# Optimization experiments

Measured on AMD Instinct MI355X. Metric: run time of the kernel, lower is better.

Reference implementation:

```python
import jax, jax.numpy as jnp
import numpy as np

TOKENS, DIM, DIM_OUT, R, ALPHA = 8192, 4096, 4096, 16, 32
SCALE = ALPHA / R  # 2.0


def setup_inputs() -> dict:
    key = jax.random.key(0)
    k1, k2, k3, k4, k5 = jax.random.split(key, 5)
    x = jax.random.normal(k1, (TOKENS, DIM), dtype=jnp.float32)
    A = jax.random.normal(k2, (DIM, R), dtype=jnp.float32)
    B = jax.random.normal(k3, (R, DIM_OUT), dtype=jnp.float32) * 0.02
    W = jax.random.normal(k4, (DIM_OUT, DIM), dtype=jnp.float32) * 0.02  # base Linear weight
    b = jax.random.normal(k5, (DIM_OUT,), dtype=jnp.float32)
    return {"x": x, "A": A, "B": B, "W": W, "b": b}


def reference(x, A, B, W, b):
    # LoRA path: x @ (A @ B) * scale, computed in the efficient low-rank order
    # (mathematically identical to materializing the full-rank weight).
    lora = ((x @ A) @ B) * SCALE              # [tokens, dim_out]
    base = x @ W.T + b                         # wrapped base Linear forward
    return lora + base
```

## Files before the change

kernel.cpp:

```cpp
#include <hip/hip_runtime.h>
#include <hip/hip_bf16.h>
#include <stdint.h>

#define TOKENS   8192
#define DIM      4096
#define DIM_OUT  4096
#define LORA_R   16
#define LORA_SCALE 2.0f

typedef __bf16 bf16_t;
typedef __attribute__((ext_vector_type(8))) __bf16 bfrag;
typedef __attribute__((ext_vector_type(4))) float f32x4;

__device__ __forceinline__ void gload_lds16(const bf16_t* gsrc, bf16_t* ldst) {
    __builtin_amdgcn_global_load_lds(
        (const __attribute__((address_space(1))) uint32_t*)(const void*)gsrc,
        (__attribute__((address_space(3))) uint32_t*)(void*)ldst,
        16, 0, 0);
}

#define CAST_BLOCKS 2048
__global__ void prep_kernel(const float* __restrict__ x, bf16_t* __restrict__ xb,
                            const float* __restrict__ W, const float* __restrict__ A,
                            const float* __restrict__ B, bf16_t* __restrict__ Wt) {
    if (blockIdx.x < CAST_BLOCKS) {
        const int total = TOKENS * DIM / 8;
        for (int i = blockIdx.x * blockDim.x + threadIdx.x; i < total;
             i += CAST_BLOCKS * 256) {
            const float4* p = reinterpret_cast<const float4*>(x + (size_t)i * 8);
            float4 v0 = p[0], v1 = p[1];
            union { bf16_t o[8]; uint4 u; } pk;
            pk.o[0] = (bf16_t)v0.x; pk.o[1] = (bf16_t)v0.y;
            pk.o[2] = (bf16_t)v0.z; pk.o[3] = (bf16_t)v0.w;
            pk.o[4] = (bf16_t)v1.x; pk.o[5] = (bf16_t)v1.y;
            pk.o[6] = (bf16_t)v1.z; pk.o[7] = (bf16_t)v1.w;
            *reinterpret_cast<uint4*>(xb + (size_t)i * 8) = pk.u;
        }
    } else {
        int idx = (blockIdx.x - CAST_BLOCKS) * blockDim.x + threadIdx.x;
        int k0 = (idx & 511) << 3;
        int n0 = (idx >> 9) << 2;

        float bn[4][16];
#pragma unroll
        for (int r = 0; r < 16; ++r) {
            float4 bv = *reinterpret_cast<const float4*>(B + (size_t)r * DIM_OUT + n0);
            bn[0][r] = bv.x; bn[1][r] = bv.y; bn[2][r] = bv.z; bn[3][r] = bv.w;
        }
        float ab[4][8];
#pragma unroll
        for (int j = 0; j < 8; ++j) {
            const float4* ap = reinterpret_cast<const float4*>(A + (size_t)(k0 + j) * LORA_R);
            float4 a0 = ap[0], a1 = ap[1], a2 = ap[2], a3 = ap[3];
            float av[16] = {a0.x,a0.y,a0.z,a0.w,a1.x,a1.y,a1.z,a1.w,
                            a2.x,a2.y,a2.z,a2.w,a3.x,a3.y,a3.z,a3.w};
#pragma unroll
            for (int n = 0; n < 4; ++n) {
                float s = 0.f;
#pragma unroll
                for (int r = 0; r < 16; ++r) s += av[r] * bn[n][r];
                ab[n][j] = s;
            }
        }
#pragma unroll
        for (int n = 0; n < 4; ++n) {
            const float4* wp = reinterpret_cast<const float4*>(W + (size_t)(n0 + n) * DIM + k0);
            float4 w0 = wp[0], w1 = wp[1];
            float wv[8] = {w0.x,w0.y,w0.z,w0.w,w1.x,w1.y,w1.z,w1.w};
            union { bf16_t o[8]; uint4 u; } pk;
#pragma unroll
            for (int j = 0; j < 8; ++j) pk.o[j] = (bf16_t)(wv[j] + LORA_SCALE * ab[n][j]);
            *reinterpret_cast<uint4*>(Wt + (size_t)(n0 + n) * DIM + k0) = pk.u;
        }
    }
}

#define BM 256
#define BN 256
#define BK 64
#define MB_BLKS (TOKENS / BM)
#define NB_BLKS (DIM_OUT / BN)
#define NT      (DIM / BK)

#define SB0() __builtin_amdgcn_sched_barrier(0)
#define VMWAIT_(n) asm volatile("s_waitcnt vmcnt(" #n ")" ::: "memory")
#define VMWAIT(n) VMWAIT_(n)
#define TILEBAR() do { SB0(); VMWAIT(0); __builtin_amdgcn_s_barrier(); SB0(); } while (0)

__global__ __launch_bounds__(512, 2) void gemm_kernel(
    const bf16_t* __restrict__ Xb, const bf16_t* __restrict__ Wt,
    const float* __restrict__ bias, float* __restrict__ C)
{
    __shared__ __align__(16) bf16_t sA[2][BM][BK];
    __shared__ __align__(16) bf16_t sB[2][BN][BK];

    const int nwg = MB_BLKS * NB_BLKS;
    int bid = blockIdx.x;
    int swz = (bid & 7) * (nwg >> 3) + (bid >> 3);
    int bm = swz / NB_BLKS;
    int bn = swz % NB_BLKS;

    const int tid  = threadIdx.x;
    const int lane = tid & 63;
    const int wid  = tid >> 6;
    const int wr   = wid >> 2;
    const int wc   = wid & 3;

    const int srow = tid >> 3;
    const int scol = (tid & 7) * 8;
    const int koff = (((tid & 7) ^ ((tid >> 3) & 7)) * 8);
    const bf16_t* Ag = Xb + (size_t)(bm * BM + srow) * DIM + koff;
    const bf16_t* Bg = Wt + (size_t)(bn * BN + srow) * DIM + koff;

#define STAGE_A(dd, kt) do { \
    const bf16_t* s_ = Ag + (size_t)(kt) * BK; \
    bf16_t* d_ = &sA[dd][srow][scol]; \
    gload_lds16(s_,                     d_); \
    gload_lds16(s_ + (size_t)64  * DIM, d_ + 64  * BK); \
    gload_lds16(s_ + (size_t)128 * DIM, d_ + 128 * BK); \
    gload_lds16(s_ + (size_t)192 * DIM, d_ + 192 * BK); \
} while (0)

#define STAGE_B(dd, kt) do { \
    const bf16_t* s_ = Bg + (size_t)(kt) * BK; \
    bf16_t* d_ = &sB[dd][srow][scol]; \
    gload_lds16(s_,                     d_); \
    gload_lds16(s_ + (size_t)64  * DIM, d_ + 64  * BK); \
    gload_lds16(s_ + (size_t)128 * DIM, d_ + 128 * BK); \
    gload_lds16(s_ + (size_t)192 * DIM, d_ + 192 * BK); \
} while (0)

    const int q     = lane & 7;
    const int kslot = lane >> 4;
    const int r15   = lane & 15;
    const int cK0   = ((kslot    ) ^ q) * 8;
    const int cK1   = ((kslot + 4) ^ q) * 8;
    const int arow0 = wr * 128 + r15;
    const int brow0 = wc * 64  + r15;

    f32x4 acc[8][4] = {};
    bfrag aLo[4][2], aHi[4][2], bLo[2][2], bHi[2][2];

#define READ_A4(dst, dd, mb) do { \
    _Pragma("unroll") \
    for (int m_ = 0; m_ < 4; ++m_) { \
        dst[m_][0] = *reinterpret_cast<const bfrag*>(&sA[dd][arow0 + (mb + m_) * 16][cK0]); \
        dst[m_][1] = *reinterpret_cast<const bfrag*>(&sA[dd][arow0 + (mb + m_) * 16][cK1]); \
    } \
} while (0)

#define READ_B2(dst, dd, nb) do { \
    _Pragma("unroll") \
    for (int n_ = 0; n_ < 2; ++n_) { \
        dst[n_][0] = *reinterpret_cast<const bfrag*>(&sB[dd][brow0 + (nb + n_) * 16][cK0]); \
        dst[n_][1] = *reinterpret_cast<const bfrag*>(&sB[dd][brow0 + (nb + n_) * 16][cK1]); \
    } \
} while (0)

#define MFMA_Q(Af, Bf, mb, nb) do { \
    __builtin_amdgcn_s_setprio(1); \
    _Pragma("unroll") \
    for (int m_ = 0; m_ < 4; ++m_) \
    _Pragma("unroll") \
    for (int n_ = 0; n_ < 2; ++n_) \
    _Pragma("unroll") \
    for (int ks_ = 0; ks_ < 2; ++ks_) \
        acc[mb + m_][nb + n_] = __builtin_amdgcn_mfma_f32_16x16x32_bf16( \
            Af[m_][ks_], Bf[n_][ks_], acc[mb + m_][nb + n_], 0, 0, 0); \
    __builtin_amdgcn_s_setprio(0); \
} while (0)

#define TILE1(d, ktn, S) do { \
    if (S) { STAGE_A((d) ^ 1, ktn); STAGE_B((d) ^ 1, ktn); } \
    READ_A4(aLo, d, 0); READ_B2(bLo, d, 0); READ_B2(bHi, d, 2); READ_A4(aHi, d, 4); \
    MFMA_Q(aLo, bLo, 0, 0); MFMA_Q(aLo, bHi, 0, 2); \
    MFMA_Q(aHi, bHi, 4, 2); MFMA_Q(aHi, bLo, 4, 0); \
    TILEBAR(); \
} while (0)

    STAGE_A(0, 0); STAGE_B(0, 0);
    TILEBAR();

    for (int it = 0; it < NT / 2 - 1; ++it) {
        int t = 2 * it;
        TILE1(0, t + 1, true);
        TILE1(1, t + 2, true);
    }
    TILE1(0, 63, true);
    TILE1(1, 0, false);

    int row0 = bm * BM + wr * 128 + (lane >> 4) * 4;
    int col0 = bn * BN + wc * 64 + r15;
#pragma unroll
    for (int n = 0; n < 4; ++n) {
        int c = col0 + n * 16;
        float bv = bias[c];
#pragma unroll
        for (int m = 0; m < 8; ++m) {
            int r = row0 + m * 16;
#pragma unroll
            for (int j = 0; j < 4; ++j)
                C[(size_t)(r + j) * DIM_OUT + c] = acc[m][n][j] + bv;
        }
    }
}

extern "C" void kernel_launch(void* const* d_in, const int* in_sizes, int n_in,
                              void* d_out, int out_size, void* d_ws, size_t ws_size,
                              hipStream_t stream) {
    const float* x = (const float*)d_in[0];
    const float* A = (const float*)d_in[1];
    const float* B = (const float*)d_in[2];
    const float* W = (const float*)d_in[3];
    const float* b = (const float*)d_in[4];
    float* out = (float*)d_out;

    bf16_t* xb = (bf16_t*)d_ws;
    bf16_t* Wt = (bf16_t*)((char*)d_ws + (size_t)TOKENS * DIM * 2);

    prep_kernel<<<CAST_BLOCKS + 2048, 256, 0, stream>>>(x, xb, W, A, B, Wt);
    gemm_kernel<<<MB_BLKS * NB_BLKS, 512, 0, stream>>>(xb, Wt, b, out);
}
```

Measured before the change: 335.7 us.

## Use BK=32 with four LDS buffers and partial vmcnt waits

```diff
diff --git a/kernel.cpp b/kernel.cpp
--- a/kernel.cpp
+++ b/kernel.cpp
@@ -77,7 +77,7 @@
 
 #define BM 256
 #define BN 256
-#define BK 64
+#define BK 32
 #define MB_BLKS (TOKENS / BM)
 #define NB_BLKS (DIM_OUT / BN)
 #define NT      (DIM / BK)
@@ -85,14 +85,13 @@
 #define SB0() __builtin_amdgcn_sched_barrier(0)
 #define VMWAIT_(n) asm volatile("s_waitcnt vmcnt(" #n ")" ::: "memory")
 #define VMWAIT(n) VMWAIT_(n)
-#define TILEBAR() do { SB0(); VMWAIT(0); __builtin_amdgcn_s_barrier(); SB0(); } while (0)
 
 __global__ __launch_bounds__(512, 2) void gemm_kernel(
     const bf16_t* __restrict__ Xb, const bf16_t* __restrict__ Wt,
     const float* __restrict__ bias, float* __restrict__ C)
 {
-    __shared__ __align__(16) bf16_t sA[2][BM][BK];
-    __shared__ __align__(16) bf16_t sB[2][BN][BK];
+    __shared__ __align__(16) bf16_t sA[4][BM][BK];
+    __shared__ __align__(16) bf16_t sB[4][BN][BK];
 
     const int nwg = MB_BLKS * NB_BLKS;
     int bid = blockIdx.x;
@@ -106,88 +105,68 @@
     const int wr   = wid >> 2;
     const int wc   = wid & 3;
 
-    const int srow = tid >> 3;
-    const int scol = (tid & 7) * 8;
-    const int koff = (((tid & 7) ^ ((tid >> 3) & 7)) * 8);
+    const int srow = tid >> 2;
+    const int slin = (tid & 3) * 8;
+    const int koff = (((tid & 3) ^ ((tid >> 3) & 3)) * 8);
     const bf16_t* Ag = Xb + (size_t)(bm * BM + srow) * DIM + koff;
     const bf16_t* Bg = Wt + (size_t)(bn * BN + srow) * DIM + koff;
 
-#define STAGE_A(dd, kt) do { \
+#define STAGE_A(sb, kt) do { \
     const bf16_t* s_ = Ag + (size_t)(kt) * BK; \
-    bf16_t* d_ = &sA[dd][srow][scol]; \
-    gload_lds16(s_,                     d_); \
-    gload_lds16(s_ + (size_t)64  * DIM, d_ + 64  * BK); \
-    gload_lds16(s_ + (size_t)128 * DIM, d_ + 128 * BK); \
-    gload_lds16(s_ + (size_t)192 * DIM, d_ + 192 * BK); \
+    gload_lds16(s_,                     &sA[sb][srow][slin]); \
+    gload_lds16(s_ + (size_t)128 * DIM, &sA[sb][128 + srow][slin]); \
 } while (0)
 
-#define STAGE_B(dd, kt) do { \
+#define STAGE_B(sb, kt) do { \
     const bf16_t* s_ = Bg + (size_t)(kt) * BK; \
-    bf16_t* d_ = &sB[dd][srow][scol]; \
-    gload_lds16(s_,                     d_); \
-    gload_lds16(s_ + (size_t)64  * DIM, d_ + 64  * BK); \
-    gload_lds16(s_ + (size_t)128 * DIM, d_ + 128 * BK); \
-    gload_lds16(s_ + (size_t)192 * DIM, d_ + 192 * BK); \
+    gload_lds16(s_,                     &sB[sb][srow][slin]); \
+    gload_lds16(s_ + (size_t)128 * DIM, &sB[sb][128 + srow][slin]); \
 } while (0)
 
-    const int q     = lane & 7;
-    const int kslot = lane >> 4;
-    const int r15   = lane & 15;
-    const int cK0   = ((kslot    ) ^ q) * 8;
-    const int cK1   = ((kslot + 4) ^ q) * 8;
+    const int r15  = lane & 15;
+    const int cK   = (((lane >> 4) ^ ((r15 >> 1) & 3))) * 8;
     const int arow0 = wr * 128 + r15;
     const int brow0 = wc * 64  + r15;
 
     f32x4 acc[8][4] = {};
-    bfrag aLo[4][2], aHi[4][2], bLo[2][2], bHi[2][2];
-
-#define READ_A4(dst, dd, mb) do { \
-    _Pragma("unroll") \
-    for (int m_ = 0; m_ < 4; ++m_) { \
-        dst[m_][0] = *reinterpret_cast<const bfrag*>(&sA[dd][arow0 + (mb + m_) * 16][cK0]); \
-        dst[m_][1] = *reinterpret_cast<const bfrag*>(&sA[dd][arow0 + (mb + m_) * 16][cK1]); \
-    } \
+    bfrag a[8], b[4];
+
+#define TILE(rb, sb, ktn, S, VM) do { \
+    if (S) { STAGE_A(sb, ktn); STAGE_B(sb, ktn); } \
+    _Pragma("unroll") \
+    for (int n_ = 0; n_ < 4; ++n_) \
+        b[n_] = *reinterpret_cast<const bfrag*>(&sB[rb][brow0 + n_ * 16][cK]); \
+    _Pragma("unroll") \
+    for (int m_ = 0; m_ < 8; ++m_) \
+        a[m_] = *reinterpret_cast<const bfrag*>(&sA[rb][arow0 + m_ * 16][cK]); \
+    __builtin_amdgcn_s_setprio(1); \
+    _Pragma("unroll") \
+    for (int m_ = 0; m_ < 8; ++m_) \
+    _Pragma("unroll") \
+    for (int n_ = 0; n_ < 4; ++n_) \
+        acc[m_][n_] = __builtin_amdgcn_mfma_f32_16x16x32_bf16( \
+            a[m_], b[n_], acc[m_][n_], 0, 0, 0); \
+    __builtin_amdgcn_s_setprio(0); \
+    SB0(); VMWAIT(VM); __builtin_amdgcn_s_barrier(); SB0(); \
 } while (0)
 
-#define READ_B2(dst, dd, nb) do { \
-    _Pragma("unroll") \
-    for (int n_ = 0; n_ < 2; ++n_) { \
-        dst[n_][0] = *reinterpret_cast<const bfrag*>(&sB[dd][brow0 + (nb + n_) * 16][cK0]); \
-        dst[n_][1] = *reinterpret_cast<const bfrag*>(&sB[dd][brow0 + (nb + n_) * 16][cK1]); \
-    } \
-} while (0)
-
-#define MFMA_Q(Af, Bf, mb, nb) do { \
-    __builtin_amdgcn_s_setprio(1); \
-    _Pragma("unroll") \
-    for (int m_ = 0; m_ < 4; ++m_) \
-    _Pragma("unroll") \
-    for (int n_ = 0; n_ < 2; ++n_) \
-    _Pragma("unroll") \
-    for (int ks_ = 0; ks_ < 2; ++ks_) \
-        acc[mb + m_][nb + n_] = __builtin_amdgcn_mfma_f32_16x16x32_bf16( \
-            Af[m_][ks_], Bf[n_][ks_], acc[mb + m_][nb + n_], 0, 0, 0); \
-    __builtin_amdgcn_s_setprio(0); \
-} while (0)
-
-#define TILE1(d, ktn, S) do { \
-    if (S) { STAGE_A((d) ^ 1, ktn); STAGE_B((d) ^ 1, ktn); } \
-    READ_A4(aLo, d, 0); READ_B2(bLo, d, 0); READ_B2(bHi, d, 2); READ_A4(aHi, d, 4); \
-    MFMA_Q(aLo, bLo, 0, 0); MFMA_Q(aLo, bHi, 0, 2); \
-    MFMA_Q(aHi, bHi, 4, 2); MFMA_Q(aHi, bLo, 4, 0); \
-    TILEBAR(); \
-} while (0)
-
     STAGE_A(0, 0); STAGE_B(0, 0);
-    TILEBAR();
-
-    for (int it = 0; it < NT / 2 - 1; ++it) {
-        int t = 2 * it;
-        TILE1(0, t + 1, true);
-        TILE1(1, t + 2, true);
+    STAGE_A(1, 1); STAGE_B(1, 1);
+    STAGE_A(2, 2); STAGE_B(2, 2);
+    VMWAIT(8);
+    __builtin_amdgcn_s_barrier(); SB0();
+
+    for (int it = 0; it < NT / 4 - 1; ++it) {
+        int t = 4 * it;
+        TILE(0, 2, t + 2, true, 4);
+        TILE(1, 3, t + 3, true, 4);
+        TILE(2, 0, t + 4, true, 4);
+        TILE(3, 1, t + 5, true, 4);
     }
-    TILE1(0, 63, true);
-    TILE1(1, 0, false);
+    TILE(0, 2, 126, true,  4);
+    TILE(1, 3, 127, true,  4);
+    TILE(2, 0, 0,   false, 0);
+    TILE(3, 1, 0,   false, 0);
 
     int row0 = bm * BM + wr * 128 + (lane >> 4) * 4;
     int col0 = bn * BN + wc * 64 + r15;
```

Result: no change. 339.7 us (+1.2%).
